# Performance work log

Measured on AMD Instinct MI355X. Metric: run time of the kernel, lower is better.

## Reference

```python
import jax, jax.numpy as jnp
import numpy as np

B, S, D, H, E, K = 2, 2048, 1024, 4096, 8, 2

def setup_inputs() -> dict:
    key = jax.random.key(0)
    ks = jax.random.split(key, 6)
    scale = 0.02
    return {
        "x": jax.random.normal(ks[0], (B, S, D), dtype=jnp.float32),
        "router_w": jax.random.normal(ks[1], (E, D), dtype=jnp.float32) * scale,
        "w1": jax.random.normal(ks[2], (E, D, H), dtype=jnp.float32) * scale,
        "b1": jnp.zeros((E, H), dtype=jnp.float32),
        "w2": jax.random.normal(ks[3], (E, H, D), dtype=jnp.float32) * scale,
        "b2": jnp.zeros((E, D), dtype=jnp.float32),
    }

def reference(x, router_w, w1, b1, w2, b2):
    # eval mode: no router noise (is_training=False), dropout inactive
    T = B * S
    x_flat = x.reshape(T, D)
    router_logits = x_flat @ router_w.T                      # [T,E]
    router_probs = jax.nn.softmax(router_logits, axis=-1)
    top_k_probs, top_k_idx = jax.lax.top_k(router_probs, K)  # [T,K]
    top_k_probs = top_k_probs / (top_k_probs.sum(-1, keepdims=True) + 1e-8)
    # dense combine weights [T,E]: prob for chosen experts, 0 elsewhere
    combine = jnp.zeros((T, E), dtype=x.dtype).at[
        jnp.arange(T)[:, None], top_k_idx].add(top_k_probs)
    # run every token through every expert (dense masked MoE, same math)
    h = jax.nn.gelu(jnp.einsum('td,edh->eth', x_flat, w1) + b1[:, None, :],
                    approximate=False)                        # [E,T,H]
    y = jnp.einsum('eth,ehd->etd', h, w2) + b2[:, None, :]    # [E,T,D]
    out = jnp.einsum('etd,te->td', y, combine).reshape(B, S, D)
    # load-balancing loss
    mean_probs = router_probs.mean(axis=0)                    # [E]
    frac = jax.nn.one_hot(top_k_idx, E, dtype=x.dtype).sum(axis=(0, 1)) / (T * K)
    load_balancing_loss = jnp.sum(mean_probs * frac) * E
    return out, load_balancing_loss
```

## Files before the change

kernel.cpp:

```cpp
#include <hip/hip_runtime.h>
#include <cstdint>
#include <cstddef>

#define T_TOKENS 4096
#define DDIM     1024
#define HDIM     4096
#define NEXP     8
#define MAXROWS  9216
#define MAXTILES 72

typedef __attribute__((ext_vector_type(8))) short bf16x8;
typedef __attribute__((ext_vector_type(4))) float f32x4;

__device__ __forceinline__ unsigned short f2bf(float x) {
  union { float f; unsigned int u; } v; v.f = x;
  unsigned int r = v.u + 0x7fffu + ((v.u >> 16) & 1u);
  return (unsigned short)(r >> 16);
}
__device__ __forceinline__ float bf2f(unsigned short b) {
  union { unsigned int u; float f; } v; v.u = ((unsigned int)b) << 16;
  return v.f;
}
__device__ __forceinline__ void async_cp16(const void* g, void* l) {
  __builtin_amdgcn_global_load_lds(
      (__attribute__((address_space(1))) void*)g,
      (__attribute__((address_space(3))) void*)l, 16, 0, 0);
}
__device__ __forceinline__ int swz(int r) { return (r ^ (r >> 3)) & 7; }

__global__ __launch_bounds__(256)
void moe_router(const float* __restrict__ x, const float* __restrict__ rw,
                int* __restrict__ tk_idx, float* __restrict__ tk_prob,
                int* __restrict__ counts, float* __restrict__ meanprob) {
  __shared__ float sp[NEXP];
  __shared__ int   sc[NEXP];
  const int tid = threadIdx.x;
  if (tid < NEXP) { sp[tid] = 0.f; sc[tid] = 0; }
  __syncthreads();
  const int wave = tid >> 6, lane = tid & 63;
  const int t = blockIdx.x * 4 + wave;
  float acc[NEXP] = {};
  for (int i = 0; i < 16; ++i) {
    const int d = i * 64 + lane;
    const float xv = x[(size_t)t * DDIM + d];
#pragma unroll
    for (int e = 0; e < NEXP; ++e) acc[e] += xv * rw[e * DDIM + d];
  }
#pragma unroll
  for (int e = 0; e < NEXP; ++e) {
#pragma unroll
    for (int m = 32; m >= 1; m >>= 1) acc[e] += __shfl_xor(acc[e], m);
  }
  if (lane == 0) {
    float mx = acc[0];
#pragma unroll
    for (int e = 1; e < NEXP; ++e) mx = fmaxf(mx, acc[e]);
    float p[NEXP], s = 0.f;
#pragma unroll
    for (int e = 0; e < NEXP; ++e) { p[e] = expf(acc[e] - mx); s += p[e]; }
    const float inv = 1.f / s;
#pragma unroll
    for (int e = 0; e < NEXP; ++e) p[e] *= inv;
    int i0 = 0;
#pragma unroll
    for (int e = 1; e < NEXP; ++e) if (p[e] > p[i0]) i0 = e;
    int i1 = (i0 == 0) ? 1 : 0;
#pragma unroll
    for (int e = 0; e < NEXP; ++e) if (e != i0 && p[e] > p[i1]) i1 = e;
    const float dn = 1.f / (p[i0] + p[i1] + 1e-8f);
    tk_idx[2 * t] = i0; tk_idx[2 * t + 1] = i1;
    tk_prob[2 * t] = p[i0] * dn; tk_prob[2 * t + 1] = p[i1] * dn;
#pragma unroll
    for (int e = 0; e < NEXP; ++e) atomicAdd(&sp[e], p[e]);
    atomicAdd(&sc[i0], 1); atomicAdd(&sc[i1], 1);
  }
  __syncthreads();
  if (tid < NEXP) {
    atomicAdd(&counts[tid], sc[tid]);
    atomicAdd(&meanprob[tid], sp[tid]);
  }
}

__global__ __launch_bounds__(256)
void moe_assign(const int* __restrict__ counts, const int* __restrict__ tk_idx,
                int* __restrict__ slot_of, int* __restrict__ off_out,
                const float* __restrict__ meanprob, float* __restrict__ loss_out) {
  const int e = blockIdx.x;
  const int tid = threadIdx.x;
  int off[NEXP + 1];
  off[0] = 0;
#pragma unroll
  for (int i = 0; i < NEXP; ++i) off[i + 1] = off[i] + ((counts[i] + 127) & ~127);
  if (e == 0 && tid == 0) {
#pragma unroll
    for (int i = 0; i <= NEXP; ++i) off_out[i] = off[i];
    float loss = 0.f;
#pragma unroll
    for (int i = 0; i < NEXP; ++i) loss += meanprob[i] * (float)counts[i];
    loss_out[0] = loss * (8.f / (4096.f * 8192.f));
  }
  __shared__ int wsum[4];
  int cursor = off[e];
  const int lane = tid & 63, w = tid >> 6;
  for (int i0 = 0; i0 < T_TOKENS * 2; i0 += 256) {
    const int idx = i0 + tid;
    const int match = (tk_idx[idx] == e) ? 1 : 0;
    const unsigned long long b = __ballot(match);
    if (lane == 0) wsum[w] = __popcll(b);
    __syncthreads();
    int wbase = cursor;
    for (int j = 0; j < 4; ++j) { if (j == w) break; wbase += wsum[j]; }
    if (match) slot_of[idx] = wbase + __popcll(b & ((1ull << lane) - 1ull));
    cursor += wsum[0] + wsum[1] + wsum[2] + wsum[3];
    __syncthreads();
  }
}

__global__ __launch_bounds__(256)
void moe_scatter(const float* __restrict__ x, const int* __restrict__ slot_of,
                 unsigned short* __restrict__ Xg) {
  const int wave = threadIdx.x >> 6, lane = threadIdx.x & 63;
  const int t = blockIdx.x * 4 + wave;
  const int pos0 = slot_of[2 * t], pos1 = slot_of[2 * t + 1];
#pragma unroll
  for (int i = 0; i < 4; ++i) {
    const int d4 = (i * 64 + lane) * 4;
    const float4 f = *(const float4*)(x + (size_t)t * DDIM + d4);
    ushort4 u;
    u.x = f2bf(f.x); u.y = f2bf(f.y); u.z = f2bf(f.z); u.w = f2bf(f.w);
    *(ushort4*)(Xg + (size_t)pos0 * DDIM + d4) = u;
    *(ushort4*)(Xg + (size_t)pos1 * DDIM + d4) = u;
  }
}

__global__ __launch_bounds__(256)
void moe_convw(const float* __restrict__ src, unsigned short* __restrict__ dst,
               int K, int N) {
  __shared__ unsigned short tile[64][72];
  const int n0 = blockIdx.x * 64, k0 = blockIdx.y * 64, e = blockIdx.z;
  const int tid = threadIdx.x;
  const float* s = src + ((size_t)e * K + k0) * N + n0;
#pragma unroll
  for (int p = 0; p < 4; ++p) {
    const int r = p * 16 + (tid >> 4);
    const int c = (tid & 15) * 4;
    const float4 f = *(const float4*)(s + (size_t)r * N + c);
    tile[r][c + 0] = f2bf(f.x); tile[r][c + 1] = f2bf(f.y);
    tile[r][c + 2] = f2bf(f.z); tile[r][c + 3] = f2bf(f.w);
  }
  __syncthreads();
#pragma unroll
  for (int p = 0; p < 4; ++p) {
    const int n = p * 16 + (tid >> 4);
    const int k = (tid & 15) * 4;
    ushort4 u;
    u.x = tile[k + 0][n]; u.y = tile[k + 1][n];
    u.z = tile[k + 2][n]; u.w = tile[k + 3][n];
    *(ushort4*)(dst + ((size_t)e * N + n0 + n) * K + k0 + k) = u;
  }
}

template <int KTOT, int N, bool GELU>
__global__ __launch_bounds__(256, 4)
void moe_gemm(const unsigned short* __restrict__ A,
              const unsigned short* __restrict__ Bt,
              const float* __restrict__ bias, unsigned short* __restrict__ C,
              const int* __restrict__ off) {
  __shared__ unsigned short As[128 * 64];
  __shared__ unsigned short Bs[128 * 64];

  const int tiles = off[8] >> 7;
  const int mt = blockIdx.x;
  if (mt >= tiles) return;
  const int row0 = mt << 7;
  int e = 0;
  while (off[e + 1] <= row0) ++e;
  const int n0 = blockIdx.y * 128;

  const unsigned short* Ap = A + (size_t)row0 * KTOT;
  const unsigned short* Bp = Bt + ((size_t)e * N + n0) * KTOT;
  const float* biasp = bias + (size_t)e * N + n0;

  const int tid = threadIdx.x;
  const int wave = tid >> 6, lane = tid & 63;
  const int qd = lane >> 4, ln = lane & 15;
  const int wm = (wave & 1) << 6, wn = (wave >> 1) << 6;

  f32x4 acc[4][4] = {};

  for (int kb = 0; kb < KTOT / 64; ++kb) {
    __syncthreads();
#pragma unroll
    for (int rr = 0; rr < 4; ++rr) {
      const int p = rr * 256 + tid;
      const int r = p >> 3, q = p & 7;
      const int gq = q ^ swz(r);
      const size_t goff = (size_t)r * KTOT + kb * 64 + gq * 8;
      unsigned short* lbase = (unsigned short*)((p & ~63) * 16);
      async_cp16(Ap + goff, As + (size_t)(p & ~63) * 8);
      async_cp16(Bp + goff, Bs + (size_t)(p & ~63) * 8);
      (void)lbase;
    }
    __syncthreads();
#pragma unroll
    for (int s = 0; s < 2; ++s) {
      bf16x8 a[4], b[4];
#pragma unroll
      for (int i = 0; i < 4; ++i) {
        const int m = wm + i * 16 + ln;
        const int pos = (s * 4 + qd) ^ swz(m);
        a[i] = *(const bf16x8*)(As + ((size_t)m * 8 + pos) * 8);
      }
#pragma unroll
      for (int j = 0; j < 4; ++j) {
        const int n = wn + j * 16 + ln;
        const int pos = (s * 4 + qd) ^ swz(n);
        b[j] = *(const bf16x8*)(Bs + ((size_t)n * 8 + pos) * 8);
      }
#pragma unroll
      for (int i = 0; i < 4; ++i)
#pragma unroll
        for (int j = 0; j < 4; ++j)
          acc[i][j] = __builtin_amdgcn_mfma_f32_16x16x32_bf16(a[i], b[j], acc[i][j], 0, 0, 0);
    }
  }

#pragma unroll
  for (int j = 0; j < 4; ++j) {
    const int cn = wn + j * 16 + ln;
    const float bv = biasp[cn];
#pragma unroll
    for (int i = 0; i < 4; ++i) {
#pragma unroll
      for (int r = 0; r < 4; ++r) {
        const int gm = row0 + wm + i * 16 + qd * 4 + r;
        float v = acc[i][j][r] + bv;
        if (GELU) v = 0.5f * v * (1.f + erff(v * 0.70710678118654752f));
        C[(size_t)gm * N + n0 + cn] = f2bf(v);
      }
    }
  }
}

__global__ __launch_bounds__(256)
void moe_combine(const unsigned short* __restrict__ Ys,
                 const float* __restrict__ tk_prob,
                 const int* __restrict__ slot_of, float* __restrict__ out) {
  const int wave = threadIdx.x >> 6, lane = threadIdx.x & 63;
  const int t = blockIdx.x * 4 + wave;
  const float p0 = tk_prob[2 * t], p1 = tk_prob[2 * t + 1];
  const int s0 = slot_of[2 * t], s1 = slot_of[2 * t + 1];
#pragma unroll
  for (int i = 0; i < 4; ++i) {
    const int d = (i * 64 + lane) * 4;
    const ushort4 a = *(const ushort4*)(Ys + (size_t)s0 * DDIM + d);
    const ushort4 b = *(const ushort4*)(Ys + (size_t)s1 * DDIM + d);
    float4 o;
    o.x = p0 * bf2f(a.x) + p1 * bf2f(b.x);
    o.y = p0 * bf2f(a.y) + p1 * bf2f(b.y);
    o.z = p0 * bf2f(a.z) + p1 * bf2f(b.z);
    o.w = p0 * bf2f(a.w) + p1 * bf2f(b.w);
    *(float4*)(out + (size_t)t * DDIM + d) = o;
  }
}

extern "C" void kernel_launch(void* const* d_in, const int* in_sizes, int n_in,
                              void* d_out, int out_size, void* d_ws, size_t ws_size,
                              hipStream_t stream) {
  const float* x  = (const float*)d_in[0];
  const float* rw = (const float*)d_in[1];
  const float* w1 = (const float*)d_in[2];
  const float* b1 = (const float*)d_in[3];
  const float* w2 = (const float*)d_in[4];
  const float* b2 = (const float*)d_in[5];
  float* out = (float*)d_out;

  char* w = (char*)d_ws;
  int*   counts   = (int*)(w + 0);
  int*   off      = (int*)(w + 64);
  float* meanprob = (float*)(w + 128);
  int*   tk_idx   = (int*)(w + 256);
  float* tk_prob  = (float*)(w + 33024);
  int*   slot_of  = (int*)(w + 65792);
  unsigned short* Xg = (unsigned short*)(w + 98816);
  unsigned short* Ys = Xg;
  unsigned short* Hs = (unsigned short*)(w + 18973184);
  unsigned short* Bt = (unsigned short*)(w + 94470656);

  hipMemsetAsync(d_ws, 0, 256, stream);
  moe_router<<<dim3(T_TOKENS / 4), dim3(256), 0, stream>>>(x, rw, tk_idx, tk_prob,
                                                           counts, meanprob);
  moe_assign<<<dim3(NEXP), dim3(256), 0, stream>>>(counts, tk_idx, slot_of, off,
                                                   meanprob,
                                                   out + (size_t)T_TOKENS * DDIM);
  moe_scatter<<<dim3(T_TOKENS / 4), dim3(256), 0, stream>>>(x, slot_of, Xg);
  moe_convw<<<dim3(HDIM / 64, DDIM / 64, NEXP), dim3(256), 0, stream>>>(w1, Bt, DDIM, HDIM);
  moe_gemm<DDIM, HDIM, true><<<dim3(MAXTILES, HDIM / 128), dim3(256), 0, stream>>>(
      Xg, Bt, b1, Hs, off);
  moe_convw<<<dim3(DDIM / 64, HDIM / 64, NEXP), dim3(256), 0, stream>>>(w2, Bt, HDIM, DDIM);
  moe_gemm<HDIM, DDIM, false><<<dim3(MAXTILES, DDIM / 128), dim3(256), 0, stream>>>(
      Hs, Bt, b2, Ys, off);
  moe_combine<<<dim3(T_TOKENS / 4), dim3(256), 0, stream>>>(Ys, tk_prob, slot_of, out);
}
```

Measured before the change: 590.1 us.

## Split-K the second expert GEMM and vectorize weight transpose conversion

The down-projection GEMM (K=4096, N=1024) launches only 72x8 blocks, so it is split along K into two halves writing separate bf16 partial outputs. The combine kernel then sums both partials when the workspace is large enough. The weight convert/transpose kernel is also reworked so each thread loads a 4x4 block and writes wider 16-byte stores. Split-K doubles the second GEMM's output traffic and rounds each partial to bf16, which adds a little numerical error.

Result: slower. 611.0 us (+3.5%).

```diff
diff --git a/kernel.cpp b/kernel.cpp
--- a/kernel.cpp
+++ b/kernel.cpp
@@ -136,36 +136,41 @@
 __global__ __launch_bounds__(256)
 void moe_convw(const float* __restrict__ src, unsigned short* __restrict__ dst,
                int K, int N) {
-  __shared__ unsigned short tile[64][72];
+  __shared__ unsigned short LT[64 * 72];
   const int n0 = blockIdx.x * 64, k0 = blockIdx.y * 64, e = blockIdx.z;
   const int tid = threadIdx.x;
-  const float* s = src + ((size_t)e * K + k0) * N + n0;
-#pragma unroll
-  for (int p = 0; p < 4; ++p) {
-    const int r = p * 16 + (tid >> 4);
-    const int c = (tid & 15) * 4;
-    const float4 f = *(const float4*)(s + (size_t)r * N + c);
-    tile[r][c + 0] = f2bf(f.x); tile[r][c + 1] = f2bf(f.y);
-    tile[r][c + 2] = f2bf(f.z); tile[r][c + 3] = f2bf(f.w);
+  const int c4 = (tid & 15) * 4;
+  const int r4 = (tid >> 4) * 4;
+  const float* s = src + ((size_t)e * K + k0 + r4) * N + n0 + c4;
+  float4 f[4];
+#pragma unroll
+  for (int i = 0; i < 4; ++i) f[i] = *(const float4*)(s + (size_t)i * N);
+#pragma unroll
+  for (int j = 0; j < 4; ++j) {
+    ushort4 u;
+    const float a0 = (j == 0) ? f[0].x : (j == 1) ? f[0].y : (j == 2) ? f[0].z : f[0].w;
+    const float a1 = (j == 0) ? f[1].x : (j == 1) ? f[1].y : (j == 2) ? f[1].z : f[1].w;
+    const float a2 = (j == 0) ? f[2].x : (j == 1) ? f[2].y : (j == 2) ? f[2].z : f[2].w;
+    const float a3 = (j == 0) ? f[3].x : (j == 1) ? f[3].y : (j == 2) ? f[3].z : f[3].w;
+    u.x = f2bf(a0); u.y = f2bf(a1); u.z = f2bf(a2); u.w = f2bf(a3);
+    *(ushort4*)&LT[(c4 + j) * 72 + r4] = u;
   }
   __syncthreads();
-#pragma unroll
-  for (int p = 0; p < 4; ++p) {
-    const int n = p * 16 + (tid >> 4);
-    const int k = (tid & 15) * 4;
-    ushort4 u;
-    u.x = tile[k + 0][n]; u.y = tile[k + 1][n];
-    u.z = tile[k + 2][n]; u.w = tile[k + 3][n];
-    *(ushort4*)(dst + ((size_t)e * N + n0 + n) * K + k0 + k) = u;
-  }
+  const int n = tid >> 2, kc = (tid & 3) * 16;
+  unsigned short* drow = dst + ((size_t)e * N + n0 + n) * K + k0 + kc;
+  const uint4 v0 = *(const uint4*)&LT[n * 72 + kc];
+  const uint4 v1 = *(const uint4*)&LT[n * 72 + kc + 8];
+  *(uint4*)(drow) = v0;
+  *(uint4*)(drow + 8) = v1;
 }
 
 template <int KTOT, int N, bool GELU>
 __global__ __launch_bounds__(256, 4)
 void moe_gemm(const unsigned short* __restrict__ A,
               const unsigned short* __restrict__ Bt,
-              const float* __restrict__ bias, unsigned short* __restrict__ C,
-              const int* __restrict__ off) {
+              const float* __restrict__ bias,
+              unsigned short* __restrict__ C0, unsigned short* __restrict__ C1,
+              const int* __restrict__ off, int kbn) {
   __shared__ unsigned short As[128 * 64];
   __shared__ unsigned short Bs[128 * 64];
 
@@ -176,6 +181,9 @@
   int e = 0;
   while (off[e + 1] <= row0) ++e;
   const int n0 = blockIdx.y * 128;
+  const int z = blockIdx.z;
+  const int kb0 = z * kbn;
+  unsigned short* C = z ? C1 : C0;
 
   const unsigned short* Ap = A + (size_t)row0 * KTOT;
   const unsigned short* Bp = Bt + ((size_t)e * N + n0) * KTOT;
@@ -188,7 +196,7 @@
 
   f32x4 acc[4][4] = {};
 
-  for (int kb = 0; kb < KTOT / 64; ++kb) {
+  for (int kb = kb0; kb < kb0 + kbn; ++kb) {
     __syncthreads();
 #pragma unroll
     for (int rr = 0; rr < 4; ++rr) {
@@ -196,10 +204,8 @@
       const int r = p >> 3, q = p & 7;
       const int gq = q ^ swz(r);
       const size_t goff = (size_t)r * KTOT + kb * 64 + gq * 8;
-      unsigned short* lbase = (unsigned short*)((p & ~63) * 16);
       async_cp16(Ap + goff, As + (size_t)(p & ~63) * 8);
       async_cp16(Bp + goff, Bs + (size_t)(p & ~63) * 8);
-      (void)lbase;
     }
     __syncthreads();
 #pragma unroll
@@ -225,10 +231,11 @@
     }
   }
 
+  const bool addb = (z == 0);
 #pragma unroll
   for (int j = 0; j < 4; ++j) {
     const int cn = wn + j * 16 + ln;
-    const float bv = biasp[cn];
+    const float bv = addb ? biasp[cn] : 0.f;
 #pragma unroll
     for (int i = 0; i < 4; ++i) {
 #pragma unroll
@@ -243,9 +250,11 @@
 }
 
 __global__ __launch_bounds__(256)
-void moe_combine(const unsigned short* __restrict__ Ys,
+void moe_combine(const unsigned short* __restrict__ Ys0,
+                 const unsigned short* __restrict__ Ys1,
                  const float* __restrict__ tk_prob,
-                 const int* __restrict__ slot_of, float* __restrict__ out) {
+                 const int* __restrict__ slot_of, float* __restrict__ out,
+                 int use2) {
   const int wave = threadIdx.x >> 6, lane = threadIdx.x & 63;
   const int t = blockIdx.x * 4 + wave;
   const float p0 = tk_prob[2 * t], p1 = tk_prob[2 * t + 1];
@@ -253,13 +262,21 @@
 #pragma unroll
   for (int i = 0; i < 4; ++i) {
     const int d = (i * 64 + lane) * 4;
-    const ushort4 a = *(const ushort4*)(Ys + (size_t)s0 * DDIM + d);
-    const ushort4 b = *(const ushort4*)(Ys + (size_t)s1 * DDIM + d);
+    const ushort4 a = *(const ushort4*)(Ys0 + (size_t)s0 * DDIM + d);
+    const ushort4 b = *(const ushort4*)(Ys0 + (size_t)s1 * DDIM + d);
     float4 o;
     o.x = p0 * bf2f(a.x) + p1 * bf2f(b.x);
     o.y = p0 * bf2f(a.y) + p1 * bf2f(b.y);
     o.z = p0 * bf2f(a.z) + p1 * bf2f(b.z);
     o.w = p0 * bf2f(a.w) + p1 * bf2f(b.w);
+    if (use2) {
+      const ushort4 a2 = *(const ushort4*)(Ys1 + (size_t)s0 * DDIM + d);
+      const ushort4 b2 = *(const ushort4*)(Ys1 + (size_t)s1 * DDIM + d);
+      o.x += p0 * bf2f(a2.x) + p1 * bf2f(b2.x);
+      o.y += p0 * bf2f(a2.y) + p1 * bf2f(b2.y);
+      o.z += p0 * bf2f(a2.z) + p1 * bf2f(b2.z);
+      o.w += p0 * bf2f(a2.w) + p1 * bf2f(b2.w);
+    }
     *(float4*)(out + (size_t)t * DDIM + d) = o;
   }
 }
@@ -282,10 +299,12 @@
   int*   tk_idx   = (int*)(w + 256);
   float* tk_prob  = (float*)(w + 33024);
   int*   slot_of  = (int*)(w + 65792);
-  unsigned short* Xg = (unsigned short*)(w + 98816);
-  unsigned short* Ys = Xg;
-  unsigned short* Hs = (unsigned short*)(w + 18973184);
-  unsigned short* Bt = (unsigned short*)(w + 94470656);
+  unsigned short* Xg  = (unsigned short*)(w + 98816);
+  unsigned short* Ys0 = Xg;
+  unsigned short* Hs  = (unsigned short*)(w + 18973184);
+  unsigned short* Bt  = (unsigned short*)(w + 94470656);
+  unsigned short* Ys1 = (unsigned short*)(w + 161579520);
+  const int split = (ws_size >= (size_t)180453888) ? 1 : 0;
 
   hipMemsetAsync(d_ws, 0, 256, stream);
   moe_router<<<dim3(T_TOKENS / 4), dim3(256), 0, stream>>>(x, rw, tk_idx, tk_prob,
@@ -295,10 +314,16 @@
                                                    out + (size_t)T_TOKENS * DDIM);
   moe_scatter<<<dim3(T_TOKENS / 4), dim3(256), 0, stream>>>(x, slot_of, Xg);
   moe_convw<<<dim3(HDIM / 64, DDIM / 64, NEXP), dim3(256), 0, stream>>>(w1, Bt, DDIM, HDIM);
-  moe_gemm<DDIM, HDIM, true><<<dim3(MAXTILES, HDIM / 128), dim3(256), 0, stream>>>(
-      Xg, Bt, b1, Hs, off);
+  moe_gemm<DDIM, HDIM, true><<<dim3(MAXTILES, HDIM / 128, 1), dim3(256), 0, stream>>>(
+      Xg, Bt, b1, Hs, Hs, off, DDIM / 64);
   moe_convw<<<dim3(DDIM / 64, HDIM / 64, NEXP), dim3(256), 0, stream>>>(w2, Bt, HDIM, DDIM);
-  moe_gemm<HDIM, DDIM, false><<<dim3(MAXTILES, DDIM / 128), dim3(256), 0, stream>>>(
-      Hs, Bt, b2, Ys, off);
-  moe_combine<<<dim3(T_TOKENS / 4), dim3(256), 0, stream>>>(Ys, tk_prob, slot_of, out);
-}
+  if (split) {
+    moe_gemm<HDIM, DDIM, false><<<dim3(MAXTILES, DDIM / 128, 2), dim3(256), 0, stream>>>(
+        Hs, Bt, b2, Ys0, Ys1, off, HDIM / 128);
+  } else {
+    moe_gemm<HDIM, DDIM, false><<<dim3(MAXTILES, DDIM / 128, 1), dim3(256), 0, stream>>>(
+        Hs, Bt, b2, Ys0, Ys0, off, HDIM / 64);
+  }
+  moe_combine<<<dim3(T_TOKENS / 4), dim3(256), 0, stream>>>(Ys0, Ys1, tk_prob,
+                                                            slot_of, out, split);
+}
```
